# Kernel optimization log

Hardware: AMD Instinct MI355X
Metric: run time of the kernel (lower is better)

Reference implementation:

```python
import jax, jax.numpy as jnp
import numpy as np

N_NODES = 200000
N_EDGES = 3200000
N_GRAPHS = 2000
N_MAX = 256   # max nodes per graph for dense batching (mean ~100)
K = 30        # SortAggregation k


def setup_inputs() -> dict:
    key = jax.random.key(0)
    ks = jax.random.split(key, 12)
    x = jax.random.normal(ks[0], (N_NODES, 128), jnp.float32)
    edge_index = jax.random.randint(ks[1], (2, N_EDGES), 0, N_NODES, dtype=jnp.int32)
    batch = jnp.sort(jax.random.randint(ks[2], (N_NODES,), 0, N_GRAPHS, dtype=jnp.int32))
    def lin(k, i, o):
        return (jax.random.normal(k, (i, o), jnp.float32) / np.sqrt(i)).astype(jnp.float32)
    return {
        'x': x, 'edge_index': edge_index, 'batch': batch,
        'W1': lin(ks[3], 128, 32), 'b1': jnp.zeros(32, jnp.float32),
        'W2': lin(ks[4], 32, 32),  'b2': jnp.zeros(32, jnp.float32),
        'W3': lin(ks[5], 32, 32),  'b3': jnp.zeros(32, jnp.float32),
        'W4': lin(ks[6], 32, 1),   'b4': jnp.zeros(1, jnp.float32),
        'cw5': (jax.random.normal(ks[7], (16, 1, 97), jnp.float32) / np.sqrt(97)).astype(jnp.float32),
        'cb5': jnp.zeros(16, jnp.float32),
        'cw6': (jax.random.normal(ks[8], (32, 16, 5), jnp.float32) / np.sqrt(80)).astype(jnp.float32),
        'cb6': jnp.zeros(32, jnp.float32),
        'fw1': lin(ks[9], 352, 128), 'fb1': jnp.zeros(128, jnp.float32),
        'fw2': lin(ks[10], 128, 10), 'fb2': jnp.zeros(10, jnp.float32),
    }


def _gcn_conv(h, W, b, src, dst, emask):
    # PyG GCNConv: remove self-loops handled via emask (weight 0), then add
    # self-loops weight 1; symmetric normalization D^{-1/2}(A+I)D^{-1/2} X W + b
    deg = jax.ops.segment_sum(emask, dst, num_segments=N_NODES) + 1.0  # + self loop
    dis = jax.lax.rsqrt(deg)  # deg >= 1 always, no inf
    norm = dis[src] * dis[dst] * emask  # [E]
    hw = h @ W                          # [N, out]
    agg = jax.ops.segment_sum(hw[src] * norm[:, None], dst, num_segments=N_NODES)
    agg = agg + hw * (dis * dis)[:, None]  # self-loop message
    return agg + b


def _sort_pool(x, batch):
    # PyG SortAggregation(k): dense-batch with fill = min-1, sort each graph by
    # last feature channel (descending), keep top-k rows, zero out padding, flatten.
    N, D = x.shape
    ones = jnp.ones((N,), jnp.int32)
    counts = jax.ops.segment_sum(ones, batch, num_segments=N_GRAPHS)
    offsets = jnp.concatenate([jnp.zeros((1,), jnp.int32), jnp.cumsum(counts)[:-1]])
    pos = jnp.arange(N, dtype=jnp.int32) - offsets[batch]  # batch is sorted
    fill = x.min() - 1.0
    dense = jnp.full((N_GRAPHS, N_MAX, D), fill, x.dtype).at[batch, pos].set(x)
    perm = jnp.argsort(-dense[:, :, -1], axis=1)            # descending by last channel
    dense = jnp.take_along_axis(dense, perm[:, :, None], axis=1)[:, :K]  # [G, K, D]
    dense = jnp.where(dense == fill, 0.0, dense)
    return dense.reshape(N_GRAPHS, K * D)


def _conv1d(x, w, b, stride):
    y = jax.lax.conv_general_dilated(x, w, window_strides=(stride,), padding='VALID',
                                     dimension_numbers=('NCH', 'OIH', 'NCH'))
    return y + b[None, :, None]


def reference(x, edge_index, batch, W1, b1, W2, b2, W3, b3, W4, b4,
              cw5, cb5, cw6, cb6, fw1, fb1, fw2, fb2):
    src, dst = edge_index[0], edge_index[1]
    emask = (src != dst).astype(x.dtype)  # remove_self_loops

    x1 = jnp.tanh(_gcn_conv(x,  W1, b1, src, dst, emask))
    x2 = jnp.tanh(_gcn_conv(x1, W2, b2, src, dst, emask))
    x3 = jnp.tanh(_gcn_conv(x2, W3, b3, src, dst, emask))
    x4 = jnp.tanh(_gcn_conv(x3, W4, b4, src, dst, emask))
    h = jnp.concatenate([x1, x2, x3, x4], axis=-1)  # [N, 97]

    p = _sort_pool(h, batch)                 # [G, 30*97]
    p = p[:, None, :]                        # [G, 1, 2910]
    p = jax.nn.relu(_conv1d(p, cw5, cb5, 97))  # [G, 16, 30]
    G = p.shape[0]
    p = p.reshape(G, 16, 15, 2).max(axis=-1)   # MaxPool1d(2,2) -> [G, 16, 15]
    p = jax.nn.relu(_conv1d(p, cw6, cb6, 1))   # [G, 32, 11]
    p = p.reshape(G, -1)                       # [G, 352]
    out = jax.nn.relu(p @ fw1 + fb1)           # dropout is identity at inference
    return jax.nn.log_softmax(out @ fw2 + fb2, axis=-1)
```

## Files before the change

kernel.cpp:

```cpp
#include <hip/hip_runtime.h>

#define N_NODESC 200000
#define N_EDGESC 3200000
#define N_GRAPHSC 2000
#define NMAXG 256
#define TOPK 30
#define DCAT 97
#define POOLW (TOPK*DCAT)
#define BUCKW 512
#define NBUCK ((N_NODESC+BUCKW-1)/BUCKW)
#define CAP 10240
#define PCHUNK 8192
#define NPBLK ((N_EDGESC+PCHUNK-1)/PCHUNK)

typedef int  iv4 __attribute__((ext_vector_type(4)));
typedef float fv4 __attribute__((ext_vector_type(4)));

__global__ __launch_bounds__(256) void k_binit(int* __restrict__ bcur){
  int i = blockIdx.x*256 + threadIdx.x;
  if (i < NBUCK) bcur[i] = i*CAP;
}

__global__ __launch_bounds__(256) void k_part(const int* __restrict__ src, const int* __restrict__ dst,
                                              int* __restrict__ bcur, unsigned* __restrict__ pairbuf){
  __shared__ int hcnt[NBUCK];
  __shared__ int hbase[NBUCK];
  int blk = blockIdx.x, t = threadIdx.x;
  int e0 = blk*PCHUNK;
  int e1 = e0 + PCHUNK; if (e1 > N_EDGESC) e1 = N_EDGESC;
  for (int i=t;i<NBUCK;i+=256) hcnt[i]=0;
  __syncthreads();
  for (int base=e0; base<e1; base+=1024){
    int e = base + t*4;
    if (e < e1){
      iv4 d4 = __builtin_nontemporal_load((const iv4*)(dst+e));
      iv4 s4 = __builtin_nontemporal_load((const iv4*)(src+e));
      #pragma unroll
      for (int k=0;k<4;k++){
        int d = (k==0)?d4.x:(k==1)?d4.y:(k==2)?d4.z:d4.w;
        int s = (k==0)?s4.x:(k==1)?s4.y:(k==2)?s4.z:s4.w;
        if (s!=d) atomicAdd(&hcnt[d>>9],1);
      }
    }
  }
  __syncthreads();
  for (int i=t;i<NBUCK;i+=256){
    int c = hcnt[i];
    hbase[i] = c ? atomicAdd(&bcur[i],c) : 0;
    hcnt[i] = 0;
  }
  __syncthreads();
  for (int base=e0; base<e1; base+=1024){
    int e = base + t*4;
    if (e < e1){
      iv4 d4 = __builtin_nontemporal_load((const iv4*)(dst+e));
      iv4 s4 = __builtin_nontemporal_load((const iv4*)(src+e));
      #pragma unroll
      for (int k=0;k<4;k++){
        int d = (k==0)?d4.x:(k==1)?d4.y:(k==2)?d4.z:d4.w;
        int s = (k==0)?s4.x:(k==1)?s4.y:(k==2)?s4.z:s4.w;
        if (s!=d){
          int bk = d>>9;
          int p = hbase[bk] + atomicAdd(&hcnt[bk],1);
          if (p < (bk+1)*CAP) pairbuf[p] = ((unsigned)(d&511)<<18)|(unsigned)s;
        }
      }
    }
  }
}

__global__ __launch_bounds__(512) void k_bscan(const int* __restrict__ bcur, int* __restrict__ bbase){
  __shared__ int sm[512];
  int t = threadIdx.x;
  int v = (t<NBUCK)? (bcur[t]-t*CAP) : 0;
  sm[t]=v; __syncthreads();
  for (int off=1;off<512;off<<=1){
    int u = (t>=off)? sm[t-off] : 0;
    __syncthreads();
    sm[t]+=u;
    __syncthreads();
  }
  if (t<NBUCK) bbase[t] = sm[t]-v;
}

__global__ __launch_bounds__(512) void k_bsort(const unsigned* __restrict__ pairbuf, const int* __restrict__ bcur,
                                               const int* __restrict__ bbase,
                                               int* __restrict__ degc, int* __restrict__ offs,
                                               float* __restrict__ dis, int* __restrict__ csr){
  __shared__ unsigned sl[CAP];
  __shared__ int lcsr[CAP];
  __shared__ int lcnt[512];
  __shared__ int lofs[512];
  __shared__ int lcur[512];
  int b = blockIdx.x, t = threadIdx.x;
  int cnt_b = bcur[b] - b*CAP;
  if (cnt_b > CAP) cnt_b = CAP;
  const unsigned* pb = pairbuf + (size_t)b*CAP;
  for (int i=t;i<cnt_b;i+=512) sl[i] = pb[i];
  lcnt[t]=0;
  __syncthreads();
  for (int i=t;i<cnt_b;i+=512) atomicAdd(&lcnt[sl[i]>>18],1);
  __syncthreads();
  lofs[t]=lcnt[t]; __syncthreads();
  for (int off=1;off<512;off<<=1){
    int u = (t>=off)? lofs[t-off] : 0;
    __syncthreads();
    lofs[t]+=u;
    __syncthreads();
  }
  int excl = lofs[t]-lcnt[t];
  int base = bbase[b];
  int node = b*BUCKW + t;
  if (node < N_NODESC){
    degc[node] = lcnt[t];
    offs[node] = base + excl;
    dis[node]  = rsqrtf((float)lcnt[t] + 1.0f);
  }
  lcur[t]=excl;
  __syncthreads();
  for (int i=t;i<cnt_b;i+=512){
    unsigned v = sl[i];
    int p = atomicAdd(&lcur[v>>18],1);
    lcsr[p] = (int)(v & 0x3FFFFu);
  }
  __syncthreads();
  for (int i=t;i<cnt_b;i+=512) csr[base+i]=lcsr[i];
}

__global__ void k_bhist(const int* __restrict__ batch, int* __restrict__ gcount){
  int i = blockIdx.x*256 + threadIdx.x;
  if (i < N_NODESC) atomicAdd(&gcount[batch[i]],1);
}

__global__ __launch_bounds__(1024) void k_gscan(const int* __restrict__ gcount, int* __restrict__ goff){
  __shared__ int sm[1024];
  int t=threadIdx.x;
  int i0=2*t, i1=2*t+1;
  int v0 = (i0<N_GRAPHSC)? gcount[i0]:0;
  int v1 = (i1<N_GRAPHSC)? gcount[i1]:0;
  int s = v0+v1;
  sm[t]=s; __syncthreads();
  for (int off=1;off<1024;off<<=1){
    int u=(t>=off)? sm[t-off]:0;
    __syncthreads();
    sm[t]+=u;
    __syncthreads();
  }
  int excl = sm[t]-s;
  if (i0<N_GRAPHSC) goff[i0]=excl;
  if (i1<N_GRAPHSC) goff[i1]=excl+v0;
}

template<int KIN>
__global__ __launch_bounds__(256) void k_mm(const float* __restrict__ X, const float* __restrict__ W,
                                            const float* __restrict__ dis, float* __restrict__ out){
  __shared__ float xs[256*33];
  int r0 = blockIdx.x*256;
  int t = threadIdx.x;
  int r = r0 + t;
  float acc[32];
  #pragma unroll
  for (int f=0;f<32;f++) acc[f]=0.f;
  for (int kc=0; kc<KIN; kc+=32){
    __syncthreads();
    #pragma unroll
    for (int it=0; it<8; it++){
      int idx = it*256 + t;
      int row = idx>>3, c4 = idx&7;
      int gr = r0 + row;
      fv4 v = {0.f,0.f,0.f,0.f};
      if (gr < N_NODESC) v = __builtin_nontemporal_load((const fv4*)(X + (size_t)gr*KIN + kc + c4*4));
      int bofs = row*33 + c4*4;
      xs[bofs]=v.x; xs[bofs+1]=v.y; xs[bofs+2]=v.z; xs[bofs+3]=v.w;
    }
    __syncthreads();
    const float* w0 = W + kc*32;
    const float* xrow = xs + t*33;
    #pragma unroll
    for (int k=0;k<32;k++){
      float xv = xrow[k];
      #pragma unroll
      for (int f=0;f<32;f++) acc[f] = fmaf(xv, w0[k*32+f], acc[f]);
    }
  }
  if (r >= N_NODESC) return;
  float d = dis[r];
  float4* op = (float4*)(out + (size_t)r*32);
  #pragma unroll
  for (int f4=0;f4<8;f4++)
    op[f4] = make_float4(acc[4*f4]*d, acc[4*f4+1]*d, acc[4*f4+2]*d, acc[4*f4+3]*d);
}

__global__ void k_mm4(const float* __restrict__ X, const float* __restrict__ W, const float* __restrict__ dis, float* __restrict__ out){
  int r = blockIdx.x*256+threadIdx.x;
  if (r>=N_NODESC) return;
  const float4* xr = (const float4*)(X + (size_t)r*32);
  float acc=0.f;
  #pragma unroll
  for (int k4=0;k4<8;k4++){
    float4 xv = xr[k4];
    acc = fmaf(xv.x, W[k4*4+0], acc);
    acc = fmaf(xv.y, W[k4*4+1], acc);
    acc = fmaf(xv.z, W[k4*4+2], acc);
    acc = fmaf(xv.w, W[k4*4+3], acc);
  }
  out[r]=acc*dis[r];
}

__global__ __launch_bounds__(256) void k_agg(const float* __restrict__ hws, const int* __restrict__ csr,
                      const int* __restrict__ off, const int* __restrict__ cnt,
                      const float* __restrict__ dis, const float* __restrict__ bias,
                      float* __restrict__ out){
  int t = blockIdx.x*256 + threadIdx.x;
  int n = t>>5;
  if (n>=N_NODESC) return;
  int f = t&31;
  int beg = off[n], c = cnt[n];
  float a0=0.f,a1=0.f,a2=0.f,a3=0.f,a4=0.f,a5=0.f,a6=0.f,a7=0.f;
  for (int base=0; base<c; base+=32){
    int m = c-base; if (m>32) m=32;
    int idx = (f<m)? csr[beg+base+f] : 0;
    int j=0;
    for (; j+8<=m; j+=8){
      int s0=__shfl(idx,j,32),   s1=__shfl(idx,j+1,32),
          s2=__shfl(idx,j+2,32), s3=__shfl(idx,j+3,32),
          s4=__shfl(idx,j+4,32), s5=__shfl(idx,j+5,32),
          s6=__shfl(idx,j+6,32), s7=__shfl(idx,j+7,32);
      float v0=hws[(size_t)s0*32+f];
      float v1=hws[(size_t)s1*32+f];
      float v2=hws[(size_t)s2*32+f];
      float v3=hws[(size_t)s3*32+f];
      float v4=hws[(size_t)s4*32+f];
      float v5=hws[(size_t)s5*32+f];
      float v6=hws[(size_t)s6*32+f];
      float v7=hws[(size_t)s7*32+f];
      a0+=v0; a1+=v1; a2+=v2; a3+=v3; a4+=v4; a5+=v5; a6+=v6; a7+=v7;
    }
    for (; j+4<=m; j+=4){
      int s0=__shfl(idx,j,32), s1=__shfl(idx,j+1,32),
          s2=__shfl(idx,j+2,32), s3=__shfl(idx,j+3,32);
      float v0=hws[(size_t)s0*32+f];
      float v1=hws[(size_t)s1*32+f];
      float v2=hws[(size_t)s2*32+f];
      float v3=hws[(size_t)s3*32+f];
      a0+=v0; a1+=v1; a2+=v2; a3+=v3;
    }
    for (; j<m; j++){
      int s0=__shfl(idx,j,32);
      a0 += hws[(size_t)s0*32+f];
    }
  }
  float dn = dis[n];
  float sum = ((a0+a1)+(a2+a3)) + ((a4+a5)+(a6+a7));
  float v = dn*(sum+hws[(size_t)n*32+f]) + bias[f];
  out[(size_t)n*32+f] = tanhf(v);
}

__global__ void k_agg4(const float* __restrict__ hws4, const int* __restrict__ csr,
                       const int* __restrict__ off, const int* __restrict__ cnt,
                       const float* __restrict__ dis, const float* __restrict__ b4,
                       float* __restrict__ x4){
  int n = blockIdx.x*256+threadIdx.x;
  if (n>=N_NODESC) return;
  int beg=off[n], c=cnt[n];
  float a0=0.f,a1=0.f,a2=0.f,a3=0.f;
  int e=0;
  for (; e+4<=c; e+=4){
    int s0=csr[beg+e], s1=csr[beg+e+1], s2=csr[beg+e+2], s3=csr[beg+e+3];
    a0+=hws4[s0]; a1+=hws4[s1]; a2+=hws4[s2]; a3+=hws4[s3];
  }
  for (; e<c; e++) a0+=hws4[csr[beg+e]];
  float dn=dis[n];
  x4[n] = tanhf(dn*(((a0+a1)+(a2+a3))+hws4[n]) + b4[0]);
}

__global__ __launch_bounds__(256) void k_sortpool(const float* __restrict__ x1,const float* __restrict__ x2,const float* __restrict__ x3,const float* __restrict__ x4,
                           const int* __restrict__ gcount, const int* __restrict__ goff, float* __restrict__ pool){
  __shared__ float vals[NMAXG];
  __shared__ int sel[TOPK];
  int g = blockIdx.x;
  int start = goff[g];
  int cntg = gcount[g]; if (cntg>NMAXG) cntg=NMAXG;
  int t = threadIdx.x;
  float v = 0.f;
  if (t<cntg) v = x4[start+t];
  vals[t] = v;
  __syncthreads();
  if (t<cntg){
    int rank=0;
    for (int j=0;j<cntg;j++){
      float vj=vals[j];
      rank += (vj>v) || (vj==v && j<t);
    }
    if (rank<TOPK) sel[rank]=t;
  }
  __syncthreads();
  int nsel = cntg<TOPK?cntg:TOPK;
  float* pg = pool + (size_t)g*POOLW;
  for (int idx=t; idx<POOLW; idx+=256){
    int r = idx/DCAT, c = idx - r*DCAT;
    float val=0.f;
    if (r<nsel){
      int node = start + sel[r];
      if (c<32) val = x1[(size_t)node*32+c];
      else if (c<64) val = x2[(size_t)node*32+(c-32)];
      else if (c<96) val = x3[(size_t)node*32+(c-64)];
      else val = x4[node];
    }
    pg[idx]=val;
  }
}

__global__ __launch_bounds__(128) void k_head(const float* __restrict__ pool,
                       const float* __restrict__ cw5, const float* __restrict__ cb5,
                       const float* __restrict__ cw6, const float* __restrict__ cb6,
                       const float* __restrict__ fw1, const float* __restrict__ fb1,
                       const float* __restrict__ fw2, const float* __restrict__ fb2,
                       float* __restrict__ out){
  __shared__ float P[POOLW];
  __shared__ float o5[16*30];
  __shared__ float m[16*15];
  __shared__ float o6[32*11];
  __shared__ float o1[128];
  __shared__ float logits[10];
  int g=blockIdx.x, t=threadIdx.x;
  const float* pg = pool + (size_t)g*POOLW;
  for (int i=t;i<POOLW;i+=128) P[i]=pg[i];
  __syncthreads();
  for (int i=t;i<480;i+=128){
    int o=i/30, k=i-o*30;
    float acc=cb5[o];
    const float* w=cw5+o*97;
    const float* p=P+k*97;
    for(int c=0;c<97;c++) acc = fmaf(p[c], w[c], acc);
    o5[o*30+k]=fmaxf(acc,0.f);
  }
  __syncthreads();
  for (int i=t;i<240;i+=128){
    int o=i/15,k=i-o*15;
    m[i]=fmaxf(o5[o*30+2*k], o5[o*30+2*k+1]);
  }
  __syncthreads();
  for (int i=t;i<352;i+=128){
    int o2=i/11, k=i-o2*11;
    float acc=cb6[o2];
    const float* w=cw6+o2*80;
    #pragma unroll
    for(int ii=0;ii<16;ii++)
      #pragma unroll
      for(int r=0;r<5;r++)
        acc = fmaf(m[ii*15+k+r], w[ii*5+r], acc);
    o6[o2*11+k]=fmaxf(acc,0.f);
  }
  __syncthreads();
  {
    float acc=fb1[t];
    for(int i=0;i<352;i++) acc = fmaf(o6[i], fw1[i*128+t], acc);
    o1[t]=fmaxf(acc,0.f);
  }
  __syncthreads();
  if (t<10){
    float acc=fb2[t];
    for(int j=0;j<128;j++) acc = fmaf(o1[j], fw2[j*10+t], acc);
    logits[t]=acc;
  }
  __syncthreads();
  if (t==0){
    float mx=logits[0];
    for(int c=1;c<10;c++) mx=fmaxf(mx,logits[c]);
    float s=0.f;
    for(int c=0;c<10;c++) s+=expf(logits[c]-mx);
    float lse=logf(s)+mx;
    for(int c=0;c<10;c++) out[(size_t)g*10+c]=logits[c]-lse;
  }
}

extern "C" void kernel_launch(void* const* d_in, const int* in_sizes, int n_in,
                              void* d_out, int out_size, void* d_ws, size_t ws_size,
                              hipStream_t stream){
  const float* x    = (const float*)d_in[0];
  const int*   ei   = (const int*)d_in[1];
  const int*   batch= (const int*)d_in[2];
  const float* W1=(const float*)d_in[3]; const float* b1=(const float*)d_in[4];
  const float* W2=(const float*)d_in[5]; const float* b2=(const float*)d_in[6];
  const float* W3=(const float*)d_in[7]; const float* b3=(const float*)d_in[8];
  const float* W4=(const float*)d_in[9]; const float* b4=(const float*)d_in[10];
  const float* cw5=(const float*)d_in[11]; const float* cb5=(const float*)d_in[12];
  const float* cw6=(const float*)d_in[13]; const float* cb6=(const float*)d_in[14];
  const float* fw1=(const float*)d_in[15]; const float* fb1=(const float*)d_in[16];
  const float* fw2=(const float*)d_in[17]; const float* fb2=(const float*)d_in[18];
  float* out=(float*)d_out;
  const int* src = ei;
  const int* dst = ei + N_EDGESC;

  char* ws=(char*)d_ws;
  size_t o=0;
  auto alloc=[&](size_t nbytes)->char*{ char* p=ws+o; o += (nbytes+255)&~(size_t)255; return p; };
  float* dis    = (float*)alloc((size_t)N_NODESC*4);
  int*   offs   = (int*)alloc((size_t)N_NODESC*4);
  int*   degc   = (int*)alloc((size_t)N_NODESC*4);
  int*   bcur   = (int*)alloc((size_t)NBUCK*4);
  int*   bbase  = (int*)alloc((size_t)NBUCK*4);
  int*   gcount = (int*)alloc((size_t)N_GRAPHSC*4);
  int*   goff   = (int*)alloc((size_t)N_GRAPHSC*4);
  unsigned* pairbuf = (unsigned*)alloc((size_t)NBUCK*CAP*4);
  int*   csr    = (int*)alloc((size_t)N_EDGESC*4);
  float* x1 = (float*)alloc((size_t)N_NODESC*32*4);
  float* x2 = (float*)alloc((size_t)N_NODESC*32*4);
  float* x3 = (float*)alloc((size_t)N_NODESC*32*4);
  float* x4 = (float*)alloc((size_t)N_NODESC*4);
  float* hw = (float*)alloc((size_t)N_NODESC*32*4);
  float* pool = hw;

  (void)hipMemsetAsync(gcount, 0, (size_t)N_GRAPHSC*4, stream);

  int gN = (N_NODESC+255)/256;

  k_binit<<<(NBUCK+255)/256,256,0,stream>>>(bcur);
  k_part<<<NPBLK,256,0,stream>>>(src,dst,bcur,pairbuf);
  k_bscan<<<1,512,0,stream>>>(bcur,bbase);
  k_bsort<<<NBUCK,512,0,stream>>>(pairbuf,bcur,bbase,degc,offs,dis,csr);

  k_bhist<<<gN,256,0,stream>>>(batch,gcount);
  k_gscan<<<1,1024,0,stream>>>(gcount,goff);

  int gMM=(N_NODESC+7)/8;
  k_mm<128><<<gN,256,0,stream>>>(x, W1, dis, hw);
  k_agg<<<gMM,256,0,stream>>>(hw,csr,offs,degc,dis,b1,x1);
  k_mm<32><<<gN,256,0,stream>>>(x1, W2, dis, hw);
  k_agg<<<gMM,256,0,stream>>>(hw,csr,offs,degc,dis,b2,x2);
  k_mm<32><<<gN,256,0,stream>>>(x2, W3, dis, hw);
  k_agg<<<gMM,256,0,stream>>>(hw,csr,offs,degc,dis,b3,x3);
  k_mm4<<<gN,256,0,stream>>>(x3, W4, dis, hw);
  k_agg4<<<gN,256,0,stream>>>(hw,csr,offs,degc,dis,b4,x4);

  k_sortpool<<<N_GRAPHSC,256,0,stream>>>(x1,x2,x3,x4,gcount,goff,pool);
  k_head<<<N_GRAPHSC,128,0,stream>>>(pool,cw5,cb5,cw6,cb6,fw1,fb1,fw2,fb2,out);
}
```

Before: 524.6 us.

## Single-pass edge partition, fold bucket scan into bsort, unroll agg4 by 8

The partition kernel now reads each edge chunk once (half-size chunks), keeping packed pairs and local slot indices in registers instead of re-reading src/dst in a second pass. The separate single-block bucket scan kernel is removed; each bsort block computes its base by reducing the counts of earlier buckets, and bsort reads pairbuf directly from global rather than staging it in LDS. agg4 uses 8 accumulators to raise memory-level parallelism. The tradeoff is more partition blocks issuing global atomics, redundant prefix work in every bsort block, and two global reads of pairbuf per bucket.

```diff
diff --git a/kernel.cpp b/kernel.cpp
--- a/kernel.cpp
+++ b/kernel.cpp
@@ -10,7 +10,7 @@
 #define BUCKW 512
 #define NBUCK ((N_NODESC+BUCKW-1)/BUCKW)
 #define CAP 10240
-#define PCHUNK 8192
+#define PCHUNK 4096
 #define NPBLK ((N_EDGESC+PCHUNK-1)/PCHUNK)
 
 typedef int  iv4 __attribute__((ext_vector_type(4)));
@@ -29,29 +29,11 @@
   int e0 = blk*PCHUNK;
   int e1 = e0 + PCHUNK; if (e1 > N_EDGESC) e1 = N_EDGESC;
   for (int i=t;i<NBUCK;i+=256) hcnt[i]=0;
-  __syncthreads();
-  for (int base=e0; base<e1; base+=1024){
-    int e = base + t*4;
-    if (e < e1){
-      iv4 d4 = __builtin_nontemporal_load((const iv4*)(dst+e));
-      iv4 s4 = __builtin_nontemporal_load((const iv4*)(src+e));
-      #pragma unroll
-      for (int k=0;k<4;k++){
-        int d = (k==0)?d4.x:(k==1)?d4.y:(k==2)?d4.z:d4.w;
-        int s = (k==0)?s4.x:(k==1)?s4.y:(k==2)?s4.z:s4.w;
-        if (s!=d) atomicAdd(&hcnt[d>>9],1);
-      }
-    }
-  }
-  __syncthreads();
-  for (int i=t;i<NBUCK;i+=256){
-    int c = hcnt[i];
-    hbase[i] = c ? atomicAdd(&bcur[i],c) : 0;
-    hcnt[i] = 0;
-  }
-  __syncthreads();
-  for (int base=e0; base<e1; base+=1024){
-    int e = base + t*4;
+  unsigned pk[16]; unsigned meta[16];
+  __syncthreads();
+  #pragma unroll
+  for (int i=0;i<4;i++){
+    int e = e0 + i*1024 + t*4;
     if (e < e1){
       iv4 d4 = __builtin_nontemporal_load((const iv4*)(dst+e));
       iv4 s4 = __builtin_nontemporal_load((const iv4*)(src+e));
@@ -61,45 +43,51 @@
         int s = (k==0)?s4.x:(k==1)?s4.y:(k==2)?s4.z:s4.w;
         if (s!=d){
           int bk = d>>9;
-          int p = hbase[bk] + atomicAdd(&hcnt[bk],1);
-          if (p < (bk+1)*CAP) pairbuf[p] = ((unsigned)(d&511)<<18)|(unsigned)s;
-        }
+          int pl = atomicAdd(&hcnt[bk],1);
+          pk[i*4+k]   = ((unsigned)(d&511)<<18)|(unsigned)s;
+          meta[i*4+k] = ((unsigned)bk<<13)|(unsigned)pl;
+        } else meta[i*4+k] = 0xFFFFFFFFu;
       }
-    }
-  }
-}
-
-__global__ __launch_bounds__(512) void k_bscan(const int* __restrict__ bcur, int* __restrict__ bbase){
-  __shared__ int sm[512];
-  int t = threadIdx.x;
-  int v = (t<NBUCK)? (bcur[t]-t*CAP) : 0;
-  sm[t]=v; __syncthreads();
-  for (int off=1;off<512;off<<=1){
-    int u = (t>=off)? sm[t-off] : 0;
-    __syncthreads();
-    sm[t]+=u;
-    __syncthreads();
-  }
-  if (t<NBUCK) bbase[t] = sm[t]-v;
+    } else {
+      #pragma unroll
+      for (int k=0;k<4;k++) meta[i*4+k] = 0xFFFFFFFFu;
+    }
+  }
+  __syncthreads();
+  for (int i=t;i<NBUCK;i+=256){
+    int c = hcnt[i];
+    hbase[i] = c ? atomicAdd(&bcur[i],c) : 0;
+  }
+  __syncthreads();
+  #pragma unroll
+  for (int k=0;k<16;k++){
+    unsigned m = meta[k];
+    if (m != 0xFFFFFFFFu){
+      int bk = (int)(m>>13);
+      int pos = hbase[bk] + (int)(m & 0x1FFFu);
+      if (pos < (bk+1)*CAP) pairbuf[pos] = pk[k];
+    }
+  }
 }
 
 __global__ __launch_bounds__(512) void k_bsort(const unsigned* __restrict__ pairbuf, const int* __restrict__ bcur,
-                                               const int* __restrict__ bbase,
                                                int* __restrict__ degc, int* __restrict__ offs,
                                                float* __restrict__ dis, int* __restrict__ csr){
-  __shared__ unsigned sl[CAP];
   __shared__ int lcsr[CAP];
   __shared__ int lcnt[512];
   __shared__ int lofs[512];
   __shared__ int lcur[512];
+  __shared__ int red[512];
   int b = blockIdx.x, t = threadIdx.x;
-  int cnt_b = bcur[b] - b*CAP;
-  if (cnt_b > CAP) cnt_b = CAP;
+  int cnt_b = bcur[b] - b*CAP; if (cnt_b > CAP) cnt_b = CAP;
+  int pv = 0;
+  if (t < b){ int c = bcur[t]-t*CAP; if (c>CAP) c=CAP; pv = c; }
+  red[t]=pv; __syncthreads();
+  for (int off=256;off>0;off>>=1){ if (t<off) red[t]+=red[t+off]; __syncthreads(); }
+  int base = red[0];
   const unsigned* pb = pairbuf + (size_t)b*CAP;
-  for (int i=t;i<cnt_b;i+=512) sl[i] = pb[i];
-  lcnt[t]=0;
-  __syncthreads();
-  for (int i=t;i<cnt_b;i+=512) atomicAdd(&lcnt[sl[i]>>18],1);
+  lcnt[t]=0; __syncthreads();
+  for (int i=t;i<cnt_b;i+=512) atomicAdd(&lcnt[pb[i]>>18],1);
   __syncthreads();
   lofs[t]=lcnt[t]; __syncthreads();
   for (int off=1;off<512;off<<=1){
@@ -109,7 +97,6 @@
     __syncthreads();
   }
   int excl = lofs[t]-lcnt[t];
-  int base = bbase[b];
   int node = b*BUCKW + t;
   if (node < N_NODESC){
     degc[node] = lcnt[t];
@@ -119,7 +106,7 @@
   lcur[t]=excl;
   __syncthreads();
   for (int i=t;i<cnt_b;i+=512){
-    unsigned v = sl[i];
+    unsigned v = pb[i];
     int p = atomicAdd(&lcur[v>>18],1);
     lcsr[p] = (int)(v & 0x3FFFFu);
   }
@@ -263,15 +250,18 @@
   int n = blockIdx.x*256+threadIdx.x;
   if (n>=N_NODESC) return;
   int beg=off[n], c=cnt[n];
-  float a0=0.f,a1=0.f,a2=0.f,a3=0.f;
+  float a0=0.f,a1=0.f,a2=0.f,a3=0.f,a4=0.f,a5=0.f,a6=0.f,a7=0.f;
   int e=0;
-  for (; e+4<=c; e+=4){
-    int s0=csr[beg+e], s1=csr[beg+e+1], s2=csr[beg+e+2], s3=csr[beg+e+3];
+  for (; e+8<=c; e+=8){
+    int s0=csr[beg+e],   s1=csr[beg+e+1], s2=csr[beg+e+2], s3=csr[beg+e+3];
+    int s4=csr[beg+e+4], s5=csr[beg+e+5], s6=csr[beg+e+6], s7=csr[beg+e+7];
     a0+=hws4[s0]; a1+=hws4[s1]; a2+=hws4[s2]; a3+=hws4[s3];
+    a4+=hws4[s4]; a5+=hws4[s5]; a6+=hws4[s6]; a7+=hws4[s7];
   }
   for (; e<c; e++) a0+=hws4[csr[beg+e]];
   float dn=dis[n];
-  x4[n] = tanhf(dn*(((a0+a1)+(a2+a3))+hws4[n]) + b4[0]);
+  float sum = ((a0+a1)+(a2+a3)) + ((a4+a5)+(a6+a7));
+  x4[n] = tanhf(dn*(sum+hws4[n]) + b4[0]);
 }
 
 __global__ __launch_bounds__(256) void k_sortpool(const float* __restrict__ x1,const float* __restrict__ x2,const float* __restrict__ x3,const float* __restrict__ x4,
@@ -400,7 +390,6 @@
   int*   offs   = (int*)alloc((size_t)N_NODESC*4);
   int*   degc   = (int*)alloc((size_t)N_NODESC*4);
   int*   bcur   = (int*)alloc((size_t)NBUCK*4);
-  int*   bbase  = (int*)alloc((size_t)NBUCK*4);
   int*   gcount = (int*)alloc((size_t)N_GRAPHSC*4);
   int*   goff   = (int*)alloc((size_t)N_GRAPHSC*4);
   unsigned* pairbuf = (unsigned*)alloc((size_t)NBUCK*CAP*4);
@@ -418,8 +407,7 @@
 
   k_binit<<<(NBUCK+255)/256,256,0,stream>>>(bcur);
   k_part<<<NPBLK,256,0,stream>>>(src,dst,bcur,pairbuf);
-  k_bscan<<<1,512,0,stream>>>(bcur,bbase);
-  k_bsort<<<NBUCK,512,0,stream>>>(pairbuf,bcur,bbase,degc,offs,dis,csr);
+  k_bsort<<<NBUCK,512,0,stream>>>(pairbuf,bcur,degc,offs,dis,csr);
 
   k_bhist<<<gN,256,0,stream>>>(batch,gcount);
   k_gscan<<<1,1024,0,stream>>>(gcount,goff);
```

Result: faster. 507.2 us (-3.3%).
